# Optimization experiments

Measured on AMD Instinct MI355X. Metric: run time of the kernel, lower is better.

## Reference

```python
import jax, jax.numpy as jnp
import numpy as np

N_NODES = 100000
N_EDGES = 3200000
IN_CH = 512
HID_CH = 40   # 2 * out_channels
OUT_CH = 20


def setup_inputs() -> dict:
    key = jax.random.key(0)
    k1, k2, k3, k4, k5, k6 = jax.random.split(key, 6)
    x = jax.random.normal(k1, (N_NODES, IN_CH), dtype=jnp.float32)
    edge_index = jax.random.randint(k2, (2, N_EDGES), 0, N_NODES, dtype=jnp.int32)
    # Glorot-style init for GCN weights, zero bias (PyG default)
    W1 = jax.random.normal(k3, (IN_CH, HID_CH), dtype=jnp.float32) * (1.0 / np.sqrt(IN_CH))
    b1 = jnp.zeros((HID_CH,), dtype=jnp.float32)
    W2 = jax.random.normal(k4, (HID_CH, OUT_CH), dtype=jnp.float32) * (1.0 / np.sqrt(HID_CH))
    b2 = jnp.zeros((OUT_CH,), dtype=jnp.float32)
    return {"x": x, "edge_index": edge_index, "W1": W1, "b1": b1, "W2": W2, "b2": b2}


def _gcn_conv(x, src, dst, W, b):
    """PyG GCNConv: add self-loops, symmetric norm, linear, scatter-add, bias."""
    n = x.shape[0]
    loops = jnp.arange(n, dtype=src.dtype)
    src = jnp.concatenate([src, loops])
    dst = jnp.concatenate([dst, loops])
    # in-degree over A + I (self-loops guarantee deg >= 1)
    deg = jax.ops.segment_sum(jnp.ones(src.shape[0], x.dtype), dst, num_segments=n)
    dinv = jax.lax.rsqrt(deg)
    norm = dinv[src] * dinv[dst]               # [E+N]
    h = x @ W                                   # [N, out] GEMM before aggregation
    msg = h[src] * norm[:, None]                # gather + scale
    out = jax.ops.segment_sum(msg, dst, num_segments=n)  # scatter-add at targets
    return out + b


def reference(x, edge_index, W1, b1, W2, b2):
    src, dst = edge_index[0], edge_index[1]
    h = jax.nn.relu(_gcn_conv(x, src, dst, W1, b1))
    # dropout is identity in eval mode (training=False)
    return _gcn_conv(h, src, dst, W2, b2)
```

## Files before the change

### kernel.cpp

```cpp
#include <hip/hip_runtime.h>
#include <cstddef>

static constexpr int NN   = 100000;
static constexpr int NE   = 3200000;
static constexpr int CIN  = 512;
static constexpr int CHID = 40;
static constexpr int COUT = 20;

typedef float f32x4 __attribute__((ext_vector_type(4)));


__global__ __launch_bounds__(256) void k_count(const int* __restrict__ dst, int* __restrict__ cnt,
                                               int* __restrict__ rank, int n_edges4) {
  const int e4 = blockIdx.x * 256 + threadIdx.x;
  if (e4 >= n_edges4) return;
  const int4 d = ((const int4*)dst)[e4];
  int4 r;
  r.x = atomicAdd(&cnt[d.x], 1);
  r.y = atomicAdd(&cnt[d.y], 1);
  r.z = atomicAdd(&cnt[d.z], 1);
  r.w = atomicAdd(&cnt[d.w], 1);
  ((int4*)rank)[e4] = r;
}

__global__ __launch_bounds__(256) void k_scanA(const int* __restrict__ cnt, int* __restrict__ excl,
                                               int* __restrict__ bsums, float* __restrict__ dinv, int n) {
  __shared__ int sdata[256];
  const int t = threadIdx.x;
  const int base = blockIdx.x * 1024 + t * 4;
  int v[4];
#pragma unroll
  for (int j = 0; j < 4; ++j) {
    const int i = base + j;
    v[j] = (i < n) ? cnt[i] : 0;
    if (i < n) dinv[i] = rsqrtf((float)(v[j] + 1));
  }
  const int s4 = v[0] + v[1] + v[2] + v[3];
  sdata[t] = s4;
  __syncthreads();
  for (int off = 1; off < 256; off <<= 1) {
    int val = 0;
    if (t >= off) val = sdata[t - off];
    __syncthreads();
    sdata[t] += val;
    __syncthreads();
  }
  int run = sdata[t] - s4;
#pragma unroll
  for (int j = 0; j < 4; ++j) {
    const int i = base + j;
    if (i < n) excl[i] = run;
    run += v[j];
  }
  if (t == 255) bsums[blockIdx.x] = sdata[255];
}

__global__ __launch_bounds__(256) void k_scanB(int* __restrict__ bsums, int nb) {
  __shared__ int sdata[256];
  const int t = threadIdx.x;
  const int v = (t < nb) ? bsums[t] : 0;
  sdata[t] = v;
  __syncthreads();
  for (int off = 1; off < 256; off <<= 1) {
    int val = 0;
    if (t >= off) val = sdata[t - off];
    __syncthreads();
    sdata[t] += val;
    __syncthreads();
  }
  if (t < nb) bsums[t] = sdata[t] - v;
}

__global__ __launch_bounds__(256) void k_scanC(int* __restrict__ rowptr, const int* __restrict__ boff,
                                               int n, int n_edges) {
  const int i = blockIdx.x * 256 + threadIdx.x;
  if (i < n) rowptr[i] += boff[i >> 10];
  if (i == 0) rowptr[n] = n_edges;
}

__global__ __launch_bounds__(256) void k_fill(const int* __restrict__ src, const int* __restrict__ dst,
                                              const int* __restrict__ rank, const int* __restrict__ rowptr,
                                              int* __restrict__ csr_src, int n_edges4) {
  const int e4 = blockIdx.x * 256 + threadIdx.x;
  if (e4 >= n_edges4) return;
  const int4 s = ((const int4*)src)[e4];
  const int4 d = ((const int4*)dst)[e4];
  const int4 r = ((const int4*)rank)[e4];
  csr_src[rowptr[d.x] + r.x] = s.x;
  csr_src[rowptr[d.y] + r.y] = s.y;
  csr_src[rowptr[d.z] + r.z] = s.z;
  csr_src[rowptr[d.w] + r.w] = s.w;
}

__global__ __launch_bounds__(256) void k_gemm1(const float* __restrict__ x, const float* __restrict__ W,
                                               float* __restrict__ h, int n) {
  __shared__ float xt[64 * 128];
  const int t  = threadIdx.x;
  const int nd = t & 63;
  const int g  = __builtin_amdgcn_readfirstlane(t >> 6);
  const int block0 = blockIdx.x * 64;

  const int sn = t >> 5;
  const int c4 = t & 31;

  float acc[10];
#pragma unroll
  for (int j = 0; j < 10; ++j) acc[j] = 0.f;

  for (int kt = 0; kt < 4; ++kt) {
    f32x4 v[8];
#pragma unroll
    for (int r = 0; r < 8; ++r) {
      const int row = r * 8 + sn;
      int gn = block0 + row;
      if (gn >= n) gn = n - 1;
      v[r] = __builtin_nontemporal_load(
          ((const f32x4*)(x + (size_t)gn * CIN + kt * 128)) + c4);
    }
    if (kt) __syncthreads();
#pragma unroll
    for (int r = 0; r < 8; ++r) {
      const int row = r * 8 + sn;
      const int byte = row * 512 + ((c4 * 16) ^ ((row & 31) << 4));
      *(f32x4*)((char*)xt + byte) = v[r];
    }
    __syncthreads();

    const float* __restrict__ Wg = W + (size_t)kt * 128 * CHID + g * 10;
#pragma unroll 4
    for (int k4 = 0; k4 < 32; ++k4) {
      const int byte = nd * 512 + ((k4 * 16) ^ ((nd & 31) << 4));
      const f32x4 xv = *(const f32x4*)((const char*)xt + byte);
      const float* __restrict__ Wk = Wg + k4 * 4 * CHID;
#pragma unroll
      for (int j = 0; j < 10; ++j) acc[j] = fmaf(xv.x, Wk[j], acc[j]);
#pragma unroll
      for (int j = 0; j < 10; ++j) acc[j] = fmaf(xv.y, Wk[CHID + j], acc[j]);
#pragma unroll
      for (int j = 0; j < 10; ++j) acc[j] = fmaf(xv.z, Wk[2 * CHID + j], acc[j]);
#pragma unroll
      for (int j = 0; j < 10; ++j) acc[j] = fmaf(xv.w, Wk[3 * CHID + j], acc[j]);
    }
  }

  __syncthreads();
#pragma unroll
  for (int j = 0; j < 10; ++j) xt[nd * 44 + g * 10 + j] = acc[j];
  __syncthreads();
  for (int i = t; i < 640; i += 256) {
    const int row = i / 10;
    const int c   = i % 10;
    const int node = block0 + row;
    if (node < n)
      ((float4*)(h + (size_t)node * CHID))[c] = *(const float4*)&xt[row * 44 + c * 4];
  }
}

__global__ __launch_bounds__(256) void k_gemm2(const float* __restrict__ t1, const float* __restrict__ W,
                                               float* __restrict__ g, int n) {
  const int node = blockIdx.x * 256 + threadIdx.x;
  if (node >= n) return;
  const float4* __restrict__ r4 = (const float4*)(t1 + (size_t)node * CHID);
  float acc[COUT];
#pragma unroll
  for (int c = 0; c < COUT; ++c) acc[c] = 0.f;
#pragma unroll
  for (int kk = 0; kk < CHID / 4; ++kk) {
    const float4 xv = r4[kk];
    const float* __restrict__ Wk = W + kk * 4 * COUT;
#pragma unroll
    for (int c = 0; c < COUT; ++c) {
      float a = acc[c];
      a = fmaf(xv.x, Wk[c], a);
      a = fmaf(xv.y, Wk[COUT + c], a);
      a = fmaf(xv.z, Wk[2 * COUT + c], a);
      a = fmaf(xv.w, Wk[3 * COUT + c], a);
      acc[c] = a;
    }
  }
  float* __restrict__ o = g + (size_t)node * COUT;
#pragma unroll
  for (int c = 0; c < COUT; ++c) o[c] = acc[c];
}

__global__ __launch_bounds__(256) void k_agg40(const float* __restrict__ h, const int* __restrict__ rowptr,
                                               const int* __restrict__ csr_src, const float* __restrict__ dinv,
                                               const float* __restrict__ bias, float* __restrict__ out, int n) {
  const int wave = (blockIdx.x * 256 + (int)threadIdx.x) >> 6;
  const int lane = threadIdx.x & 63;
  const int sub  = lane / 20;
  const int cp   = lane % 20;
  const int node = wave * 3 + sub;
  if (sub >= 3 || node >= n) return;
  const float2* __restrict__ h2 = (const float2*)h;
  const int r0 = rowptr[node];
  const int r1 = rowptr[node + 1];
  const float dv = dinv[node];
  const float self_w = dv * dv;
  float2 acc = h2[(size_t)node * 20 + cp];
  acc.x *= self_w;
  acc.y *= self_w;
  int i = r0;
  for (; i + 4 <= r1; i += 4) {
    const int s0 = csr_src[i + 0];
    const int s1 = csr_src[i + 1];
    const int s2 = csr_src[i + 2];
    const int s3 = csr_src[i + 3];
    const float w0 = dinv[s0] * dv;
    const float w1 = dinv[s1] * dv;
    const float w2 = dinv[s2] * dv;
    const float w3 = dinv[s3] * dv;
    const float2 g0 = h2[(size_t)s0 * 20 + cp];
    const float2 g1 = h2[(size_t)s1 * 20 + cp];
    const float2 g2 = h2[(size_t)s2 * 20 + cp];
    const float2 g3 = h2[(size_t)s3 * 20 + cp];
    acc.x = fmaf(g0.x, w0, acc.x); acc.y = fmaf(g0.y, w0, acc.y);
    acc.x = fmaf(g1.x, w1, acc.x); acc.y = fmaf(g1.y, w1, acc.y);
    acc.x = fmaf(g2.x, w2, acc.x); acc.y = fmaf(g2.y, w2, acc.y);
    acc.x = fmaf(g3.x, w3, acc.x); acc.y = fmaf(g3.y, w3, acc.y);
  }
  for (; i < r1; ++i) {
    const int s = csr_src[i];
    const float w = dinv[s] * dv;
    const float2 g = h2[(size_t)s * 20 + cp];
    acc.x = fmaf(g.x, w, acc.x);
    acc.y = fmaf(g.y, w, acc.y);
  }
  const float2 bv = ((const float2*)bias)[cp];
  float2 v;
  v.x = fmaxf(acc.x + bv.x, 0.f);
  v.y = fmaxf(acc.y + bv.y, 0.f);
  ((float2*)out)[(size_t)node * 20 + cp] = v;
}

__global__ __launch_bounds__(256) void k_agg20(const float* __restrict__ h, const int* __restrict__ rowptr,
                                               const int* __restrict__ csr_src, const float* __restrict__ dinv,
                                               const float* __restrict__ bias, float* __restrict__ out, int n) {
  const int wave = (blockIdx.x * 256 + (int)threadIdx.x) >> 6;
  const int lane = threadIdx.x & 63;
  const int sub  = lane / 10;
  const int cp   = lane % 10;
  const int node = wave * 6 + sub;
  if (sub >= 6 || node >= n) return;
  const float2* __restrict__ h2 = (const float2*)h;
  const int r0 = rowptr[node];
  const int r1 = rowptr[node + 1];
  const float dv = dinv[node];
  const float self_w = dv * dv;
  float2 acc = h2[(size_t)node * 10 + cp];
  acc.x *= self_w;
  acc.y *= self_w;
  int i = r0;
  for (; i + 4 <= r1; i += 4) {
    const int s0 = csr_src[i + 0];
    const int s1 = csr_src[i + 1];
    const int s2 = csr_src[i + 2];
    const int s3 = csr_src[i + 3];
    const float w0 = dinv[s0] * dv;
    const float w1 = dinv[s1] * dv;
    const float w2 = dinv[s2] * dv;
    const float w3 = dinv[s3] * dv;
    const float2 g0 = h2[(size_t)s0 * 10 + cp];
    const float2 g1 = h2[(size_t)s1 * 10 + cp];
    const float2 g2 = h2[(size_t)s2 * 10 + cp];
    const float2 g3 = h2[(size_t)s3 * 10 + cp];
    acc.x = fmaf(g0.x, w0, acc.x); acc.y = fmaf(g0.y, w0, acc.y);
    acc.x = fmaf(g1.x, w1, acc.x); acc.y = fmaf(g1.y, w1, acc.y);
    acc.x = fmaf(g2.x, w2, acc.x); acc.y = fmaf(g2.y, w2, acc.y);
    acc.x = fmaf(g3.x, w3, acc.x); acc.y = fmaf(g3.y, w3, acc.y);
  }
  for (; i < r1; ++i) {
    const int s = csr_src[i];
    const float w = dinv[s] * dv;
    const float2 g = h2[(size_t)s * 10 + cp];
    acc.x = fmaf(g.x, w, acc.x);
    acc.y = fmaf(g.y, w, acc.y);
  }
  const float2 bv = ((const float2*)bias)[cp];
  float2 v;
  v.x = acc.x + bv.x;
  v.y = acc.y + bv.y;
  ((float2*)out)[(size_t)node * 10 + cp] = v;
}


extern "C" void kernel_launch(void* const* d_in, const int* in_sizes, int n_in,
                              void* d_out, int out_size, void* d_ws, size_t ws_size,
                              hipStream_t stream) {
  const float* x   = (const float*)d_in[0];
  const int*   ei  = (const int*)d_in[1];
  const float* W1  = (const float*)d_in[2];
  const float* b1  = (const float*)d_in[3];
  const float* W2  = (const float*)d_in[4];
  const float* b2  = (const float*)d_in[5];
  float* out = (float*)d_out;

  const int* srcp = ei;
  const int* dstp = ei + NE;

  char* ws = (char*)d_ws;
  size_t off = 0;
  auto take = [&](size_t bytes) -> char* {
    char* p = ws + off;
    off = (off + bytes + 255) & ~(size_t)255;
    return p;
  };
  int*   cnt     = (int*)take((size_t)NN * 4);
  int*   rowptr  = (int*)take((size_t)(NN + 1) * 4);
  float* dinv    = (float*)take((size_t)NN * 4);
  int*   bsums   = (int*)take(256 * 4);
  int*   rank    = (int*)take((size_t)NE * 4);
  int*   csr_src = (int*)take((size_t)NE * 4);
  float* h1      = (float*)take((size_t)NN * CHID * 4);
  float* t1      = (float*)take((size_t)NN * CHID * 4);
  float* g2      = h1;

  (void)in_sizes; (void)n_in; (void)out_size; (void)ws_size;

  hipMemsetAsync(cnt, 0, (size_t)NN * 4, stream);

  const int ne4 = NE / 4;
  k_count<<<(ne4 + 255) / 256, 256, 0, stream>>>(dstp, cnt, rank, ne4);
  const int nb = (NN + 1023) / 1024;
  k_scanA<<<nb, 256, 0, stream>>>(cnt, rowptr, bsums, dinv, NN);
  k_scanB<<<1, 256, 0, stream>>>(bsums, nb);
  k_scanC<<<(NN + 255) / 256, 256, 0, stream>>>(rowptr, bsums, NN, NE);
  k_fill<<<(ne4 + 255) / 256, 256, 0, stream>>>(srcp, dstp, rank, rowptr, csr_src, ne4);

  k_gemm1<<<(NN + 63) / 64, 256, 0, stream>>>(x, W1, h1, NN);
  const int nwaves1 = (NN + 2) / 3;
  k_agg40<<<(nwaves1 + 3) / 4, 256, 0, stream>>>(h1, rowptr, csr_src, dinv, b1, t1, NN);
  k_gemm2<<<(NN + 255) / 256, 256, 0, stream>>>(t1, W2, g2, NN);
  const int nwaves2 = (NN + 5) / 6;
  k_agg20<<<(nwaves2 + 3) / 4, 256, 0, stream>>>(g2, rowptr, csr_src, dinv, b2, out, NN);
}
```

Measured before the change: 764.1 us.

## Build CSR with chunked LDS histograms instead of global atomics

Replaces the global-atomic degree count and rank-based fill with a two-pass scheme. Edges are split into 32 chunks and nodes into 8 ranges, and each block builds an LDS histogram for its chunk and range. A merge kernel turns the per-chunk counts into exclusive offsets, and the fill pass recomputes ranks with LDS atomics. This removes contended global atomics and the rank array, at the cost of reading dst 8x per pass, a 12.8 MB per-chunk count buffer, and only 256 blocks.

```diff
diff --git a/kernel.cpp b/kernel.cpp
--- a/kernel.cpp
+++ b/kernel.cpp
@@ -7,20 +7,47 @@
 static constexpr int CHID = 40;
 static constexpr int COUT = 20;
 
+static constexpr int NCH    = 32;
+static constexpr int CHUNK_E = NE / NCH;
+static constexpr int NRANGE = 8;
+static constexpr int RANGE  = NN / NRANGE;
+
 typedef float f32x4 __attribute__((ext_vector_type(4)));
 
 
-__global__ __launch_bounds__(256) void k_count(const int* __restrict__ dst, int* __restrict__ cnt,
-                                               int* __restrict__ rank, int n_edges4) {
-  const int e4 = blockIdx.x * 256 + threadIdx.x;
-  if (e4 >= n_edges4) return;
-  const int4 d = ((const int4*)dst)[e4];
-  int4 r;
-  r.x = atomicAdd(&cnt[d.x], 1);
-  r.y = atomicAdd(&cnt[d.y], 1);
-  r.z = atomicAdd(&cnt[d.z], 1);
-  r.w = atomicAdd(&cnt[d.w], 1);
-  ((int4*)rank)[e4] = r;
+__global__ __launch_bounds__(1024) void k_histA(const int* __restrict__ dst,
+                                                int* __restrict__ cntb) {
+  __shared__ int hc[RANGE];
+  const int c  = blockIdx.x >> 3;
+  const int r0 = (blockIdx.x & 7) * RANGE;
+  for (int i = threadIdx.x; i < RANGE; i += 1024) hc[i] = 0;
+  __syncthreads();
+  const int base = c * (CHUNK_E / 4);
+  const int end  = base + CHUNK_E / 4;
+  for (int i = base + (int)threadIdx.x; i < end; i += 1024) {
+    const int4 d = ((const int4*)dst)[i];
+    if ((unsigned)(d.x - r0) < (unsigned)RANGE) atomicAdd(&hc[d.x - r0], 1);
+    if ((unsigned)(d.y - r0) < (unsigned)RANGE) atomicAdd(&hc[d.y - r0], 1);
+    if ((unsigned)(d.z - r0) < (unsigned)RANGE) atomicAdd(&hc[d.z - r0], 1);
+    if ((unsigned)(d.w - r0) < (unsigned)RANGE) atomicAdd(&hc[d.w - r0], 1);
+  }
+  __syncthreads();
+  int* __restrict__ outp = cntb + (size_t)c * NN + r0;
+  for (int i = threadIdx.x; i < RANGE; i += 1024) outp[i] = hc[i];
+}
+
+__global__ __launch_bounds__(256) void k_merge(int* __restrict__ cntb, int* __restrict__ cnt, int n) {
+  const int i = blockIdx.x * 256 + threadIdx.x;
+  if (i >= n) return;
+  int s = 0;
+#pragma unroll 8
+  for (int b = 0; b < NCH; ++b) {
+    int* p = cntb + (size_t)b * NN + i;
+    const int t = *p;
+    *p = s;
+    s += t;
+  }
+  cnt[i] = s;
 }
 
 __global__ __launch_bounds__(256) void k_scanA(const int* __restrict__ cnt, int* __restrict__ excl,
@@ -78,18 +105,39 @@
   if (i == 0) rowptr[n] = n_edges;
 }
 
-__global__ __launch_bounds__(256) void k_fill(const int* __restrict__ src, const int* __restrict__ dst,
-                                              const int* __restrict__ rank, const int* __restrict__ rowptr,
-                                              int* __restrict__ csr_src, int n_edges4) {
-  const int e4 = blockIdx.x * 256 + threadIdx.x;
-  if (e4 >= n_edges4) return;
-  const int4 s = ((const int4*)src)[e4];
-  const int4 d = ((const int4*)dst)[e4];
-  const int4 r = ((const int4*)rank)[e4];
-  csr_src[rowptr[d.x] + r.x] = s.x;
-  csr_src[rowptr[d.y] + r.y] = s.y;
-  csr_src[rowptr[d.z] + r.z] = s.z;
-  csr_src[rowptr[d.w] + r.w] = s.w;
+__global__ __launch_bounds__(1024) void k_histFill(const int* __restrict__ src,
+                                                   const int* __restrict__ dst,
+                                                   const int* __restrict__ rowptr,
+                                                   const int* __restrict__ cntb,
+                                                   int* __restrict__ csr_src) {
+  __shared__ int hc[RANGE];
+  const int c  = blockIdx.x >> 3;
+  const int r0 = (blockIdx.x & 7) * RANGE;
+  for (int i = threadIdx.x; i < RANGE; i += 1024) hc[i] = 0;
+  __syncthreads();
+  const int* __restrict__ cbo = cntb + (size_t)c * NN;
+  const int base = c * (CHUNK_E / 4);
+  const int end  = base + CHUNK_E / 4;
+  for (int i = base + (int)threadIdx.x; i < end; i += 1024) {
+    const int4 d = ((const int4*)dst)[i];
+    const int4 s = ((const int4*)src)[i];
+    if ((unsigned)(d.x - r0) < (unsigned)RANGE) {
+      const int rk = atomicAdd(&hc[d.x - r0], 1);
+      csr_src[rowptr[d.x] + cbo[d.x] + rk] = s.x;
+    }
+    if ((unsigned)(d.y - r0) < (unsigned)RANGE) {
+      const int rk = atomicAdd(&hc[d.y - r0], 1);
+      csr_src[rowptr[d.y] + cbo[d.y] + rk] = s.y;
+    }
+    if ((unsigned)(d.z - r0) < (unsigned)RANGE) {
+      const int rk = atomicAdd(&hc[d.z - r0], 1);
+      csr_src[rowptr[d.z] + cbo[d.z] + rk] = s.z;
+    }
+    if ((unsigned)(d.w - r0) < (unsigned)RANGE) {
+      const int rk = atomicAdd(&hc[d.w - r0], 1);
+      csr_src[rowptr[d.w] + cbo[d.w] + rk] = s.w;
+    }
+  }
 }
 
 __global__ __launch_bounds__(256) void k_gemm1(const float* __restrict__ x, const float* __restrict__ W,
@@ -309,7 +357,7 @@
   int*   rowptr  = (int*)take((size_t)(NN + 1) * 4);
   float* dinv    = (float*)take((size_t)NN * 4);
   int*   bsums   = (int*)take(256 * 4);
-  int*   rank    = (int*)take((size_t)NE * 4);
+  int*   cntb    = (int*)take((size_t)NCH * NN * 4);
   int*   csr_src = (int*)take((size_t)NE * 4);
   float* h1      = (float*)take((size_t)NN * CHID * 4);
   float* t1      = (float*)take((size_t)NN * CHID * 4);
@@ -317,15 +365,14 @@
 
   (void)in_sizes; (void)n_in; (void)out_size; (void)ws_size;
 
-  hipMemsetAsync(cnt, 0, (size_t)NN * 4, stream);
-
-  const int ne4 = NE / 4;
-  k_count<<<(ne4 + 255) / 256, 256, 0, stream>>>(dstp, cnt, rank, ne4);
   const int nb = (NN + 1023) / 1024;
+
+  k_histA<<<NCH * NRANGE, 1024, 0, stream>>>(dstp, cntb);
+  k_merge<<<(NN + 255) / 256, 256, 0, stream>>>(cntb, cnt, NN);
   k_scanA<<<nb, 256, 0, stream>>>(cnt, rowptr, bsums, dinv, NN);
   k_scanB<<<1, 256, 0, stream>>>(bsums, nb);
   k_scanC<<<(NN + 255) / 256, 256, 0, stream>>>(rowptr, bsums, NN, NE);
-  k_fill<<<(ne4 + 255) / 256, 256, 0, stream>>>(srcp, dstp, rank, rowptr, csr_src, ne4);
+  k_histFill<<<NCH * NRANGE, 1024, 0, stream>>>(srcp, dstp, rowptr, cntb, csr_src);
 
   k_gemm1<<<(NN + 63) / 64, 256, 0, stream>>>(x, W1, h1, NN);
   const int nwaves1 = (NN + 2) / 3;
```

Result: faster. 689.0 us (-9.8%).
